# Kernel optimization log

Measured on AMD Instinct MI355X. Metric: run time of the kernel, lower is better.

Reference implementation:

```python
import jax
jax.config.update("jax_enable_x64", True)
import jax.numpy as jnp
import numpy as np

FMIX32_C1 = 2246822507
FMIX32_C2 = 3266489909
POS_C1 = 668265261
POS_C2 = 374761393
SEED = 608135816
TILE = 8192
N_WORDS = 67108864  # 64M uint32 words = 256 MB


def _fmix32(x):
    # MurmurHash3 fmix32 finalizer on uint32 (wrapping arithmetic)
    x = x ^ (x >> 16)
    x = x * jnp.uint32(FMIX32_C1)
    x = x ^ (x >> 13)
    x = x * jnp.uint32(FMIX32_C2)
    x = x ^ (x >> 16)
    return x


def _rotl32(x, r):
    return (x << r) | (x >> (32 - r))


def setup_inputs() -> dict:
    key = jax.random.key(0)
    input_words = jax.random.randint(key, (N_WORDS,), 0, 2**31 - 1, dtype=jnp.int32)
    return {"input_words": input_words}


def _hash_tiles(input_words):
    v = input_words.view(jnp.uint32) if input_words.dtype != jnp.uint32 else input_words
    v = jax.lax.bitcast_convert_type(input_words, jnp.uint32)
    n = v.shape[0]
    n_tiles = (n + TILE - 1) // TILE
    n_pad = n_tiles * TILE
    v = jnp.pad(v, (0, n_pad - n))  # padded words hash to 0 via mask below
    v = v.reshape(n_tiles, TILE)

    s1 = jnp.uint32(SEED & 0xFFFFFFFF)
    s2 = jnp.uint32((SEED * 2654435761 ^ 3735928559) & 0xFFFFFFFF)
    posA = jnp.uint32(POS_C1)
    posB = jnp.uint32(POS_C2)

    idx = jnp.arange(n_pad, dtype=jnp.uint32).reshape(n_tiles, TILE)
    m = idx < jnp.uint32(n)

    # Python precedence in the kernel: (iu*posA + s1) ^ rotl(iu, 15)
    p1 = (idx * posA + s1) ^ _rotl32(idx, 15)
    p2 = (idx * posB + s2) ^ _rotl32(idx, 13)

    k1 = jnp.where(m, _fmix32(v ^ p1), jnp.uint32(0))
    k2 = jnp.where(m, _fmix32(v ^ p2), jnp.uint32(0))

    h1 = jnp.sum(k1, axis=1, dtype=jnp.uint32)  # wrapping per-tile reduction
    h2 = jnp.sum(k2, axis=1, dtype=jnp.uint32)

    nbytes = jnp.uint32((n * 4) & 0xFFFFFFFF)
    h1 = _fmix32(h1 ^ nbytes)
    h2 = _fmix32(h2 ^ nbytes)

    out = (h1.astype(jnp.uint64) << 32) | h2.astype(jnp.uint64)
    return jax.lax.bitcast_convert_type(out, jnp.int64)  # torch returns int64


def reference(input_words) -> jnp.ndarray:
    return _hash_tiles(input_words)
```

## Files before the change

### kernel.cpp

```cpp
#include <hip/hip_runtime.h>
#include <stdint.h>


static constexpr uint32_t FMIX_C1 = 2246822507u;
static constexpr uint32_t FMIX_C2 = 3266489909u;
static constexpr uint32_t POS_A   = 668265261u;
static constexpr uint32_t POS_B   = 374761393u;
static constexpr uint32_t S1      = 608135816u;
static constexpr uint32_t S2      = (608135816u * 2654435761u) ^ 3735928559u;

__device__ __forceinline__ uint32_t fmix32(uint32_t x) {
    x ^= x >> 16;
    x *= FMIX_C1;
    x ^= x >> 13;
    x *= FMIX_C2;
    x ^= x >> 16;
    return x;
}

__device__ __forceinline__ uint32_t rotl32(uint32_t x, uint32_t r) {
    return (x << r) | (x >> (32u - r));
}

template <bool PAIRS>
__global__ __launch_bounds__(256) void hash_tiles_kernel(
        const uint32_t* __restrict__ in, uint32_t* __restrict__ out,
        uint32_t nbytes) {
    const uint32_t gid  = blockIdx.x * 256u + threadIdx.x;
    const uint32_t tile = gid >> 6;
    const uint32_t lane = threadIdx.x & 63u;
    const uint32_t base = tile << 13;

    const uint4* __restrict__ vin =
        reinterpret_cast<const uint4*>(in + base) + lane;

    uint32_t acc1 = 0u, acc2 = 0u;
    uint32_t iw = base + (lane << 2);
    uint32_t mA = iw * POS_A + S1;
    uint32_t mB = iw * POS_B + S2;
    const uint32_t stepA = 256u * POS_A;
    const uint32_t stepB = 256u * POS_B;

    #pragma unroll 4
    for (int r = 0; r < 32; ++r) {
        uint4 v = vin[r << 6];
        #pragma unroll
        for (int j = 0; j < 4; ++j) {
            uint32_t w = (j == 0) ? v.x : (j == 1) ? v.y : (j == 2) ? v.z : v.w;
            uint32_t ij = iw + (uint32_t)j;
            if (PAIRS) {
                uint32_t p1 = (mA + (uint32_t)j * POS_A) ^ rotl32(ij, 15);
                acc1 += fmix32(w ^ p1);
            }
            uint32_t p2 = (mB + (uint32_t)j * POS_B) ^ rotl32(ij, 13);
            acc2 += fmix32(w ^ p2);
        }
        iw += 256u; mA += stepA; mB += stepB;
    }

    #pragma unroll
    for (int off = 32; off > 0; off >>= 1) {
        if (PAIRS) acc1 += (uint32_t)__shfl_xor((int)acc1, off, 64);
        acc2 += (uint32_t)__shfl_xor((int)acc2, off, 64);
    }

    if (lane == 0) {
        uint32_t h2 = fmix32(acc2 ^ nbytes);
        if (PAIRS) {
            uint32_t h1 = fmix32(acc1 ^ nbytes);
            uint2 packed;
            packed.x = h2;
            packed.y = h1;
            reinterpret_cast<uint2*>(out)[tile] = packed;
        } else {
            out[tile] = h2;
        }
    }
}

extern "C" void kernel_launch(void* const* d_in, const int* in_sizes, int n_in,
                              void* d_out, int out_size, void* d_ws, size_t ws_size,
                              hipStream_t stream) {
    const uint32_t* in = (const uint32_t*)d_in[0];
    uint32_t* out = (uint32_t*)d_out;

    const uint32_t n       = (uint32_t)in_sizes[0];
    const uint32_t n_tiles = n >> 13;
    const uint32_t nbytes  = n << 2;

    dim3 block(256);
    dim3 grid(n_tiles >> 2);

    if ((uint32_t)out_size >= 2u * n_tiles) {
        hipLaunchKernelGGL(hash_tiles_kernel<true>, grid, block, 0, stream,
                           in, out, nbytes);
    } else {
        hipLaunchKernelGGL(hash_tiles_kernel<false>, grid, block, 0, stream,
                           in, out, nbytes);
    }
}
```

Measured before the change: 349.4 us.

## Assign one block per tile and preload all tile loads up front

Each 8192-word tile is now processed by a full 256-thread block instead of a single wavefront. Every thread issues its eight 16-byte loads before any hashing begins. Per-wave partial sums are combined through shared memory with a block barrier. The goal is more independent memory requests in flight and shorter serial per-thread loops, to raise achieved HBM bandwidth. The cost is a shared-memory reduction, a __syncthreads per block, and more registers holding the loaded vectors.

```diff
diff --git a/kernel.cpp b/kernel.cpp
--- a/kernel.cpp
+++ b/kernel.cpp
@@ -26,28 +26,32 @@
 __global__ __launch_bounds__(256) void hash_tiles_kernel(
         const uint32_t* __restrict__ in, uint32_t* __restrict__ out,
         uint32_t nbytes) {
-    const uint32_t gid  = blockIdx.x * 256u + threadIdx.x;
-    const uint32_t tile = gid >> 6;
-    const uint32_t lane = threadIdx.x & 63u;
+    const uint32_t tile = blockIdx.x;
+    const uint32_t tid  = threadIdx.x;
     const uint32_t base = tile << 13;
 
     const uint4* __restrict__ vin =
-        reinterpret_cast<const uint4*>(in + base) + lane;
+        reinterpret_cast<const uint4*>(in + base) + tid;
+
+    uint4 v[8];
+    #pragma unroll
+    for (int r = 0; r < 8; ++r) v[r] = vin[r << 8];
 
     uint32_t acc1 = 0u, acc2 = 0u;
-    uint32_t iw = base + (lane << 2);
-    uint32_t mA = iw * POS_A + S1;
-    uint32_t mB = iw * POS_B + S2;
-    const uint32_t stepA = 256u * POS_A;
-    const uint32_t stepB = 256u * POS_B;
+    const uint32_t iw0 = base + (tid << 2);
+    const uint32_t mA0 = iw0 * POS_A + S1;
+    const uint32_t mB0 = iw0 * POS_B + S2;
 
-    #pragma unroll 4
-    for (int r = 0; r < 32; ++r) {
-        uint4 v = vin[r << 6];
+    #pragma unroll
+    for (int r = 0; r < 8; ++r) {
+        const uint32_t iw = iw0 + (uint32_t)(r * 1024);
+        const uint32_t mA = mA0 + (uint32_t)(r * 1024) * POS_A;
+        const uint32_t mB = mB0 + (uint32_t)(r * 1024) * POS_B;
         #pragma unroll
         for (int j = 0; j < 4; ++j) {
-            uint32_t w = (j == 0) ? v.x : (j == 1) ? v.y : (j == 2) ? v.z : v.w;
-            uint32_t ij = iw + (uint32_t)j;
+            const uint32_t w  = (j == 0) ? v[r].x : (j == 1) ? v[r].y
+                              : (j == 2) ? v[r].z : v[r].w;
+            const uint32_t ij = iw + (uint32_t)j;
             if (PAIRS) {
                 uint32_t p1 = (mA + (uint32_t)j * POS_A) ^ rotl32(ij, 15);
                 acc1 += fmix32(w ^ p1);
@@ -55,7 +59,6 @@
             uint32_t p2 = (mB + (uint32_t)j * POS_B) ^ rotl32(ij, 13);
             acc2 += fmix32(w ^ p2);
         }
-        iw += 256u; mA += stepA; mB += stepB;
     }
 
     #pragma unroll
@@ -64,10 +67,20 @@
         acc2 += (uint32_t)__shfl_xor((int)acc2, off, 64);
     }
 
-    if (lane == 0) {
-        uint32_t h2 = fmix32(acc2 ^ nbytes);
+    __shared__ uint32_t red1[4], red2[4];
+    const uint32_t wv = tid >> 6;
+    if ((tid & 63u) == 0u) {
+        red2[wv] = acc2;
+        if (PAIRS) red1[wv] = acc1;
+    }
+    __syncthreads();
+
+    if (tid == 0) {
+        uint32_t a2 = red2[0] + red2[1] + red2[2] + red2[3];
+        uint32_t h2 = fmix32(a2 ^ nbytes);
         if (PAIRS) {
-            uint32_t h1 = fmix32(acc1 ^ nbytes);
+            uint32_t a1 = red1[0] + red1[1] + red1[2] + red1[3];
+            uint32_t h1 = fmix32(a1 ^ nbytes);
             uint2 packed;
             packed.x = h2;
             packed.y = h1;
@@ -89,7 +102,7 @@
     const uint32_t nbytes  = n << 2;
 
     dim3 block(256);
-    dim3 grid(n_tiles >> 2);
+    dim3 grid(n_tiles);
 
     if ((uint32_t)out_size >= 2u * n_tiles) {
         hipLaunchKernelGGL(hash_tiles_kernel<true>, grid, block, 0, stream,
```

New measurement: 351.2 us. Within noise of the previous version (+0.5%).
